# Performance work log

Hardware: AMD Instinct MI355X
Metric: run time of the kernel (lower is better)

Reference implementation:

```python
import jax, jax.numpy as jnp
import numpy as np

V = 50000      # node_num
E = 200000     # number of edges
LN = 128       # feat_dim
S = 32         # stat_dim
C = 10         # num_class
T = 2          # propagation steps
MU = 0.9


def setup_inputs() -> dict:
    key = jax.random.key(0)
    ks = jax.random.split(key, 10)
    feat_Matrix = jax.random.normal(ks[0], (V, LN), dtype=jnp.float32)
    X_Node = jax.random.randint(ks[1], (E,), 0, V, dtype=jnp.int32)
    X_Neis = jax.random.randint(ks[2], (E,), 0, V, dtype=jnp.int32)
    # degrees >= 1 (divided by in Hw)
    dg_list = jax.random.randint(ks[3], (E,), 1, 33).astype(jnp.float32)
    sc = 0.02
    Wxi = jax.random.normal(ks[4], (2 * LN, S * S), dtype=jnp.float32) * sc
    bxi = jnp.zeros((S * S,), dtype=jnp.float32)
    Wrou = jax.random.normal(ks[5], (LN, S), dtype=jnp.float32) * sc
    brou = jnp.zeros((S,), dtype=jnp.float32)
    Wout = jax.random.normal(ks[6], (S, C), dtype=jnp.float32) * sc
    bout = jnp.zeros((C,), dtype=jnp.float32)
    return {
        "feat_Matrix": feat_Matrix, "X_Node": X_Node, "X_Neis": X_Neis,
        "dg_list": dg_list, "Wxi": Wxi, "bxi": bxi,
        "Wrou": Wrou, "brou": brou, "Wout": Wout, "bout": bout,
    }


def reference(feat_Matrix, X_Node, X_Neis, dg_list,
              Wxi, bxi, Wrou, brou, Wout, bout):
    # Gather endpoint features: X = [feat[u] || feat[v]]  -> [E, 2*LN]
    X = jnp.concatenate(
        (feat_Matrix[X_Node], feat_Matrix[X_Neis]), axis=1)

    # Xi(X): per-edge transition matrix A  [E, S, S], scaled by mu/s/deg
    A = jnp.tanh(X @ Wxi + bxi).reshape(E, S, S)
    A = A * (MU / S) / dg_list[:, None, None]
    # Rou on first chunk (= node features)  [E, S]
    b = jnp.tanh(X[:, :LN] @ Wrou + brou)

    H = jnp.zeros((V, S), dtype=feat_Matrix.dtype)
    for _ in range(T):
        He = H[X_Node]                                  # gather  [E, S]
        He = jnp.einsum('eij,ej->ei', A, He) + b        # per-edge transition
        # scatter-add per node (equivalent to AggrSum's dense mask matmul)
        H = jax.ops.segment_sum(He, X_Node, num_segments=V)

    # dropout is identity at inference
    return jax.nn.log_softmax(H @ Wout + bout, axis=-1)
```

## Files before the change

kernel.cpp:

```cpp
#include <hip/hip_runtime.h>

#define EE 200000
#define VV 50000
#define LN 128
#define KD 256
#define SS 32
#define NN 1024
#define CC 10
#define MUS 0.028125f

typedef short short8_t __attribute__((ext_vector_type(8)));
typedef float f32x4 __attribute__((ext_vector_type(4)));

__device__ __forceinline__ unsigned short f32_to_bf16_rne(float f) {
    union { float f; unsigned u; } x; x.f = f;
    unsigned r = x.u + 0x7FFFu + ((x.u >> 16) & 1u);
    return (unsigned short)(r >> 16);
}

__device__ __forceinline__ float bf16_to_f32(unsigned short h) {
    union { unsigned u; float f; } x; x.u = ((unsigned)h) << 16; return x.f;
}

__device__ __forceinline__ float tanh_fast(float x) {
    float t = __builtin_amdgcn_exp2f(x * 2.885390081777927f);
    return 1.0f - 2.0f * __builtin_amdgcn_rcpf(t + 1.0f);
}

__device__ __forceinline__ float ptanh(float x) {
    float x2 = x * x;
    return x * (27.f + x2) * __builtin_amdgcn_rcpf(27.f + 9.f * x2);
}

__device__ __forceinline__ void load_lds16(const void* g, void* l) {
    __builtin_amdgcn_global_load_lds(
        (const __attribute__((address_space(1))) unsigned int*)g,
        (__attribute__((address_space(3))) unsigned int*)l,
        16, 0, 0);
}

__global__ void k_prep(const float* __restrict__ feat, unsigned short* __restrict__ featB,
                       const float* __restrict__ Wxi, unsigned short* __restrict__ WxiB,
                       const float* __restrict__ bxi, float* __restrict__ bxiT,
                       const int* __restrict__ Xn, int* __restrict__ cnt) {
    int b = blockIdx.x, tid = threadIdx.x;
    if (b < 6250) {
        int idx = b * 256 + tid;
        float4 v = ((const float4*)feat)[idx];
        ushort4 o;
        o.x = f32_to_bf16_rne(v.x); o.y = f32_to_bf16_rne(v.y);
        o.z = f32_to_bf16_rne(v.z); o.w = f32_to_bf16_rne(v.w);
        ((ushort4*)featB)[idx] = o;
    } else if (b < 7274) {
        int idx = (b - 6250) * 256 + tid;
        int k = idx >> 10, ncol = idx & 1023;
        int np = ((ncol & 31) << 5) | (ncol >> 5);
        WxiB[((size_t)(k >> 3) * NN + np) * 8 + (k & 7)] = f32_to_bf16_rne(Wxi[idx]);
    } else if (b == 7274) {
        #pragma unroll
        for (int it = 0; it < 4; ++it) {
            int i = it * 256 + tid;
            bxiT[i] = bxi[(i & 31) * 32 + (i >> 5)];
        }
    } else {
        int e = (b - 7275) * 256 + tid;
        if (e < EE) atomicAdd(&cnt[Xn[e]], 1);
    }
}

__global__ void k_scan1(const int* __restrict__ cnt, int* __restrict__ rowptr,
                        int* __restrict__ bsum) {
    __shared__ int s[256];
    int i = blockIdx.x * 256 + threadIdx.x;
    int x = (i < VV) ? cnt[i] : 0;
    s[threadIdx.x] = x; __syncthreads();
    int v = x;
    #pragma unroll
    for (int off = 1; off < 256; off <<= 1) {
        int t = (threadIdx.x >= off) ? s[threadIdx.x - off] : 0;
        __syncthreads();
        v += t; s[threadIdx.x] = v;
        __syncthreads();
    }
    if (i < VV) rowptr[i] = v - x;
    if (threadIdx.x == 255) bsum[blockIdx.x] = v;
}

__global__ void k_scan2(const int* __restrict__ bsum, int* __restrict__ boff, int nb) {
    __shared__ int s[256];
    int t = threadIdx.x;
    int x = (t < nb) ? bsum[t] : 0;
    s[t] = x; __syncthreads();
    int v = x;
    #pragma unroll
    for (int off = 1; off < 256; off <<= 1) {
        int tt = (t >= off) ? s[t - off] : 0;
        __syncthreads();
        v += tt; s[t] = v;
        __syncthreads();
    }
    boff[t] = v - x;
}

__global__ void k_scan3(int* __restrict__ rowptr, const int* __restrict__ boff,
                        int* __restrict__ cursor) {
    int i = blockIdx.x * 256 + threadIdx.x;
    if (i < VV) {
        int r = rowptr[i] + boff[blockIdx.x];
        rowptr[i] = r;
        cursor[i] = r;
    }
    if (blockIdx.x == 0 && threadIdx.x == 0) rowptr[VV] = EE;
}

__global__ void k_scatter(const int* __restrict__ Xn, int* __restrict__ cursor,
                          int* __restrict__ perm) {
    int e = blockIdx.x * 256 + threadIdx.x;
    if (e < EE) {
        int p = atomicAdd(&cursor[Xn[e]], 1);
        perm[p] = e;
    }
}

__global__ void k_h1(const float* __restrict__ feat, const float* __restrict__ Wrou,
                     const float* __restrict__ brou, const int* __restrict__ cnt,
                     float* __restrict__ H1) {
    int gid = blockIdx.x * 256 + threadIdx.x;
    int u = gid >> 5, s = gid & 31;
    const float* fr = feat + (size_t)u * LN;
    float a = brou[s];
    #pragma unroll 8
    for (int k = 0; k < LN; ++k) a += fr[k] * Wrou[k * SS + s];
    H1[gid] = (float)cnt[u] * tanh_fast(a);
}

__global__ void __launch_bounds__(256, 3)
k_edge_gemm(const unsigned short* __restrict__ featB, const unsigned short* __restrict__ WxiB,
            const int* __restrict__ Xn, const int* __restrict__ Xe,
            const float* __restrict__ dg, const float* __restrict__ bxiT,
            const int* __restrict__ perm, const float* __restrict__ H1,
            unsigned short* __restrict__ HeB) {
    __shared__ __align__(16) unsigned short Bs[2 * 8192];
    __shared__ float hs[128][33];
    __shared__ int   us[128], vs[128];
    __shared__ float scale_s[128];

    const int tid = threadIdx.x;
    const int eb = blockIdx.x * 128;

    if (tid < 128) {
        int p = eb + tid; if (p > EE - 1) p = EE - 1;
        int e0 = perm[p];
        us[tid] = Xn[e0]; vs[tid] = Xe[e0];
        scale_s[tid] = MUS / dg[e0];
    }
    __syncthreads();

    const int w = tid >> 6, lane = tid & 63;
    const int g = lane >> 4, l15 = lane & 15;
    const int row0 = w * 32;

    short8_t af[8][2];
    #pragma unroll
    for (int kk = 0; kk < 8; ++kk)
        #pragma unroll
        for (int mf = 0; mf < 2; ++mf) {
            int el = row0 + mf * 16 + l15;
            int node = (kk < 4) ? us[el] : vs[el];
            af[kk][mf] = *(const short8_t*)(featB + (size_t)node * LN + (kk & 3) * 32 + g * 8);
        }

    #pragma unroll
    for (int it = 0; it < 16; ++it) {
        int idx = it * 256 + tid;
        int el = idx >> 5, s = idx & 31;
        hs[el][s] = H1[us[el] * SS + s];
    }

    size_t qoff[4];
    int ldsoff[4];
    #pragma unroll
    for (int q = 0; q < 4; ++q) {
        int U = q * 256 + tid;
        qoff[q] = (size_t)(U >> 5) * 16384 + (size_t)(U & 31) * 16;
        ldsoff[q] = U * 16;
    }
    const char* bbase = (const char*)Bs + (g * 512 + l15 * 16);

    f32x4 he[2][2];
    #pragma unroll
    for (int mf = 0; mf < 2; ++mf)
        #pragma unroll
        for (int f = 0; f < 2; ++f)
            he[mf][f] = (f32x4){0.f, 0.f, 0.f, 0.f};

    #pragma unroll
    for (int q = 0; q < 4; ++q)
        load_lds16((const char*)WxiB + qoff[q], (char*)Bs + ldsoff[q]);
    __syncthreads();

    #pragma unroll 1
    for (int c = 0; c < 32; ++c) {
        if (c < 31) {
            const char* gs = (const char*)WxiB + (size_t)(c + 1) * 512;
            char* ld = (char*)Bs + ((c + 1) & 1) * 16384;
            #pragma unroll
            for (int q = 0; q < 4; ++q)
                load_lds16(gs + qoff[q], ld + ldsoff[q]);
        }

        const char* bslot = bbase + (c & 1) * 16384;
        f32x4 acc[2][2];
        #pragma unroll
        for (int mf = 0; mf < 2; ++mf)
            #pragma unroll
            for (int f = 0; f < 2; ++f)
                acc[mf][f] = (f32x4){0.f, 0.f, 0.f, 0.f};

        #pragma unroll
        for (int kk = 0; kk < 8; ++kk) {
            short8_t b0 = *(const short8_t*)(bslot + kk * 2048);
            short8_t b1 = *(const short8_t*)(bslot + kk * 2048 + 256);
            #pragma unroll
            for (int mf = 0; mf < 2; ++mf) {
                acc[mf][0] = __builtin_amdgcn_mfma_f32_16x16x32_bf16(af[kk][mf], b0, acc[mf][0], 0, 0, 0);
                acc[mf][1] = __builtin_amdgcn_mfma_f32_16x16x32_bf16(af[kk][mf], b1, acc[mf][1], 0, 0, 0);
            }
        }

        const float bx0 = bxiT[c * 32 + l15];
        const float bx1 = bxiT[c * 32 + 16 + l15];
        #pragma unroll
        for (int mf = 0; mf < 2; ++mf)
            #pragma unroll
            for (int r = 0; r < 4; ++r) {
                float hv = hs[row0 + mf * 16 + g * 4 + r][c];
                he[mf][0][r] += ptanh(acc[mf][0][r] + bx0) * hv;
                he[mf][1][r] += ptanh(acc[mf][1][r] + bx1) * hv;
            }

        __syncthreads();
    }

    #pragma unroll
    for (int mf = 0; mf < 2; ++mf)
        #pragma unroll
        for (int r = 0; r < 4; ++r) {
            int el = row0 + mf * 16 + g * 4 + r;
            int ep = eb + el;
            if (ep < EE) {
                float sc = scale_s[el];
                HeB[(size_t)ep * SS + l15]      = f32_to_bf16_rne(he[mf][0][r] * sc);
                HeB[(size_t)ep * SS + 16 + l15] = f32_to_bf16_rne(he[mf][1][r] * sc);
            }
        }
}

__global__ void k_reduce_out(const unsigned short* __restrict__ HeB, const int* __restrict__ rowptr,
                             const float* __restrict__ H1, const float* __restrict__ Wout,
                             const float* __restrict__ bout, float* __restrict__ out) {
    __shared__ float h2[8][33];
    __shared__ float lgS[8][10];
    __shared__ float lseS[8];
    int tid = threadIdx.x;
    int un8 = tid >> 5, s = tid & 31;
    int u = blockIdx.x * 8 + un8;
    int p0 = rowptr[u], p1 = rowptr[u + 1];
    float acc = H1[u * SS + s];
    for (int p = p0; p < p1; ++p)
        acc += bf16_to_f32(HeB[(size_t)p * SS + s]);
    h2[un8][s] = acc;
    __syncthreads();
    if (tid < 80) {
        int un = tid / 10, c = tid - un * 10;
        float a = bout[c];
        #pragma unroll
        for (int s2 = 0; s2 < SS; ++s2) a += h2[un][s2] * Wout[s2 * CC + c];
        lgS[un][c] = a;
    }
    __syncthreads();
    if (tid < 8) {
        float mx = lgS[tid][0];
        #pragma unroll
        for (int c = 1; c < CC; ++c) mx = fmaxf(mx, lgS[tid][c]);
        float se = 0.f;
        #pragma unroll
        for (int c = 0; c < CC; ++c)
            se += __builtin_amdgcn_exp2f((lgS[tid][c] - mx) * 1.4426950408889634f);
        lseS[tid] = mx + __builtin_amdgcn_logf(se) * 0.6931471805599453f;
    }
    __syncthreads();
    if (tid < 80) {
        int un = tid / 10, c = tid - un * 10;
        out[(size_t)(blockIdx.x * 8 + un) * CC + c] = lgS[un][c] - lseS[un];
    }
}

extern "C" void kernel_launch(void* const* d_in, const int* in_sizes, int n_in,
                              void* d_out, int out_size, void* d_ws, size_t ws_size,
                              hipStream_t stream) {
    const float* feat = (const float*)d_in[0];
    const int*   Xn   = (const int*)d_in[1];
    const int*   Xe   = (const int*)d_in[2];
    const float* dg   = (const float*)d_in[3];
    const float* Wxi  = (const float*)d_in[4];
    const float* bxi  = (const float*)d_in[5];
    const float* Wrou = (const float*)d_in[6];
    const float* brou = (const float*)d_in[7];
    const float* Wout = (const float*)d_in[8];
    const float* bout = (const float*)d_in[9];
    float* out = (float*)d_out;

    char* ws = (char*)d_ws;
    unsigned short* featB  = (unsigned short*)(ws);
    unsigned short* WxiB   = (unsigned short*)(ws + 12800000);
    unsigned short* HeB    = (unsigned short*)(ws + 13324288);
    float*          H1     = (float*)(ws + 26124288);
    int*            perm   = (int*)(ws + 32524288);
    int*            rowptr = (int*)(ws + 33324288);
    int*            cursor = (int*)(ws + 33524352);
    int*            cnt    = (int*)(ws + 33724352);
    float*          bxiT   = (float*)(ws + 33924352);
    int*            bsum   = (int*)(ws + 33928448);
    int*            boff   = (int*)(ws + 33929472);

    hipMemsetAsync(cnt, 0, 200000, stream);

    k_prep      <<<8057, 256, 0, stream>>>(feat, featB, Wxi, WxiB, bxi, bxiT, Xn, cnt);
    k_h1        <<<(VV * SS) / 256, 256, 0, stream>>>(feat, Wrou, brou, cnt, H1);
    k_scan1     <<<196, 256, 0, stream>>>(cnt, rowptr, bsum);
    k_scan2     <<<1, 256, 0, stream>>>(bsum, boff, 196);
    k_scan3     <<<196, 256, 0, stream>>>(rowptr, boff, cursor);
    k_scatter   <<<782, 256, 0, stream>>>(Xn, cursor, perm);
    k_edge_gemm <<<(EE + 127) / 128, 256, 0, stream>>>(featB, WxiB, Xn, Xe, dg, bxiT, perm, H1, HeB);
    k_reduce_out<<<VV / 8, 256, 0, stream>>>(HeB, rowptr, H1, Wout, bout, out);
}
```

Before: 322.4 us.

## Fuse rou into prep, single-pass lookback scan, and double edge tile per block

Moves the Rou projection into the prep kernel, storing tanh(feat@Wrou) without the degree factor; the degree is now recovered from rowptr where it is used. The three-kernel scan becomes one decoupled-lookback scan that publishes block flags through a zeroed workspace. The edge GEMM now handles 256 edges per block with four M-fragments per wave and launch bounds lowered to two blocks. It also replaces the loop-end __syncthreads with an explicit waitcnt and barrier. The aim is fewer launches and more reuse of each Wxi tile loaded into LDS, at the cost of more registers and lower occupancy, plus a lookback that relies on blocks being scheduled in order.

```diff
diff --git a/kernel.cpp b/kernel.cpp
--- a/kernel.cpp
+++ b/kernel.cpp
@@ -42,7 +42,9 @@
 __global__ void k_prep(const float* __restrict__ feat, unsigned short* __restrict__ featB,
                        const float* __restrict__ Wxi, unsigned short* __restrict__ WxiB,
                        const float* __restrict__ bxi, float* __restrict__ bxiT,
-                       const int* __restrict__ Xn, int* __restrict__ cnt) {
+                       const int* __restrict__ Xn, int* __restrict__ cnt,
+                       const float* __restrict__ Wrou, const float* __restrict__ brou,
+                       float* __restrict__ R) {
     int b = blockIdx.x, tid = threadIdx.x;
     if (b < 6250) {
         int idx = b * 256 + tid;
@@ -62,55 +64,81 @@
             int i = it * 256 + tid;
             bxiT[i] = bxi[(i & 31) * 32 + (i >> 5)];
         }
-    } else {
+    } else if (b < 8057) {
         int e = (b - 7275) * 256 + tid;
         if (e < EE) atomicAdd(&cnt[Xn[e]], 1);
-    }
-}
-
-__global__ void k_scan1(const int* __restrict__ cnt, int* __restrict__ rowptr,
-                        int* __restrict__ bsum) {
+    } else {
+        int gid = (b - 8057) * 256 + tid;
+        int u = gid >> 5, s = gid & 31;
+        const float* fr = feat + (size_t)u * LN;
+        float a = brou[s];
+        #pragma unroll 8
+        for (int k = 0; k < LN; ++k) a += fr[k] * Wrou[k * SS + s];
+        R[gid] = tanh_fast(a);
+    }
+}
+
+__global__ void __launch_bounds__(256) k_scan_lb(const int* __restrict__ cnt,
+                                                 int* __restrict__ rowptr,
+                                                 int* __restrict__ cursor,
+                                                 unsigned int* flags) {
     __shared__ int s[256];
-    int i = blockIdx.x * 256 + threadIdx.x;
+    __shared__ int bp;
+    int b = blockIdx.x, tid = threadIdx.x;
+    int i = b * 256 + tid;
     int x = (i < VV) ? cnt[i] : 0;
-    s[threadIdx.x] = x; __syncthreads();
+    s[tid] = x; __syncthreads();
     int v = x;
     #pragma unroll
     for (int off = 1; off < 256; off <<= 1) {
-        int t = (threadIdx.x >= off) ? s[threadIdx.x - off] : 0;
+        int t = (tid >= off) ? s[tid - off] : 0;
         __syncthreads();
-        v += t; s[threadIdx.x] = v;
+        v += t; s[tid] = v;
         __syncthreads();
     }
-    if (i < VV) rowptr[i] = v - x;
-    if (threadIdx.x == 255) bsum[blockIdx.x] = v;
-}
-
-__global__ void k_scan2(const int* __restrict__ bsum, int* __restrict__ boff, int nb) {
-    __shared__ int s[256];
-    int t = threadIdx.x;
-    int x = (t < nb) ? bsum[t] : 0;
-    s[t] = x; __syncthreads();
-    int v = x;
-    #pragma unroll
-    for (int off = 1; off < 256; off <<= 1) {
-        int tt = (t >= off) ? s[t - off] : 0;
-        __syncthreads();
-        v += tt; s[t] = v;
-        __syncthreads();
-    }
-    boff[t] = v - x;
-}
-
-__global__ void k_scan3(int* __restrict__ rowptr, const int* __restrict__ boff,
-                        int* __restrict__ cursor) {
-    int i = blockIdx.x * 256 + threadIdx.x;
-    if (i < VV) {
-        int r = rowptr[i] + boff[blockIdx.x];
-        rowptr[i] = r;
-        cursor[i] = r;
-    }
-    if (blockIdx.x == 0 && threadIdx.x == 0) rowptr[VV] = EE;
+    int agg = s[255];
+
+    if (b == 0) {
+        if (tid == 0) {
+            bp = 0;
+            atomicExch(&flags[0], 0x80000000u | (unsigned)agg);
+        }
+    } else {
+        if (tid == 0)
+            atomicExch(&flags[b], 0x40000000u | (unsigned)agg);
+        if (tid < 64) {
+            int lane = tid;
+            int base = b - 1;
+            int pref = 0;
+            while (true) {
+                int idx = base - lane;
+                unsigned wv;
+                if (idx >= 0) {
+                    do { wv = atomicAdd(&flags[idx], 0u); } while ((wv & 0xC0000000u) == 0u);
+                } else {
+                    wv = 0x80000000u;
+                }
+                bool isP = (wv >= 0x80000000u);
+                unsigned long long bal = __ballot(isP);
+                int Lp = bal ? __builtin_ctzll(bal) : 64;
+                int val = (int)(wv & 0x3FFFFFFFu);
+                int contrib = (lane < Lp) ? val : ((lane == Lp && bal) ? val : 0);
+                #pragma unroll
+                for (int o = 1; o < 64; o <<= 1) contrib += __shfl_xor(contrib, o);
+                pref += contrib;
+                if (bal) break;
+                base -= 64;
+            }
+            if (lane == 0) {
+                bp = pref;
+                atomicExch(&flags[b], 0x80000000u | (unsigned)(pref + agg));
+            }
+        }
+    }
+    __syncthreads();
+    int excl = v - x + bp;
+    if (i < VV) { rowptr[i] = excl; cursor[i] = excl; }
+    if (b == 0 && tid == 0) rowptr[VV] = EE;
 }
 
 __global__ void k_scatter(const int* __restrict__ Xn, int* __restrict__ cursor,
@@ -122,59 +150,49 @@
     }
 }
 
-__global__ void k_h1(const float* __restrict__ feat, const float* __restrict__ Wrou,
-                     const float* __restrict__ brou, const int* __restrict__ cnt,
-                     float* __restrict__ H1) {
-    int gid = blockIdx.x * 256 + threadIdx.x;
-    int u = gid >> 5, s = gid & 31;
-    const float* fr = feat + (size_t)u * LN;
-    float a = brou[s];
-    #pragma unroll 8
-    for (int k = 0; k < LN; ++k) a += fr[k] * Wrou[k * SS + s];
-    H1[gid] = (float)cnt[u] * tanh_fast(a);
-}
-
-__global__ void __launch_bounds__(256, 3)
+__global__ void __launch_bounds__(256, 2)
 k_edge_gemm(const unsigned short* __restrict__ featB, const unsigned short* __restrict__ WxiB,
             const int* __restrict__ Xn, const int* __restrict__ Xe,
             const float* __restrict__ dg, const float* __restrict__ bxiT,
-            const int* __restrict__ perm, const float* __restrict__ H1,
-            unsigned short* __restrict__ HeB) {
+            const int* __restrict__ perm, const float* __restrict__ R,
+            const int* __restrict__ rowptr, unsigned short* __restrict__ HeB) {
     __shared__ __align__(16) unsigned short Bs[2 * 8192];
-    __shared__ float hs[128][33];
-    __shared__ int   us[128], vs[128];
-    __shared__ float scale_s[128];
+    __shared__ float hs[256][33];
+    __shared__ int   us[256], vs[256];
+    __shared__ float scale_s[256], cs[256];
 
     const int tid = threadIdx.x;
-    const int eb = blockIdx.x * 128;
-
-    if (tid < 128) {
+    const int eb = blockIdx.x * 256;
+
+    {
         int p = eb + tid; if (p > EE - 1) p = EE - 1;
         int e0 = perm[p];
-        us[tid] = Xn[e0]; vs[tid] = Xe[e0];
+        int u = Xn[e0];
+        us[tid] = u; vs[tid] = Xe[e0];
         scale_s[tid] = MUS / dg[e0];
+        cs[tid] = (float)(rowptr[u + 1] - rowptr[u]);
     }
     __syncthreads();
 
     const int w = tid >> 6, lane = tid & 63;
     const int g = lane >> 4, l15 = lane & 15;
-    const int row0 = w * 32;
-
-    short8_t af[8][2];
+    const int row0 = w * 64;
+
+    short8_t af[8][4];
     #pragma unroll
     for (int kk = 0; kk < 8; ++kk)
         #pragma unroll
-        for (int mf = 0; mf < 2; ++mf) {
+        for (int mf = 0; mf < 4; ++mf) {
             int el = row0 + mf * 16 + l15;
             int node = (kk < 4) ? us[el] : vs[el];
             af[kk][mf] = *(const short8_t*)(featB + (size_t)node * LN + (kk & 3) * 32 + g * 8);
         }
 
     #pragma unroll
-    for (int it = 0; it < 16; ++it) {
+    for (int it = 0; it < 32; ++it) {
         int idx = it * 256 + tid;
-        int el = idx >> 5, s = idx & 31;
-        hs[el][s] = H1[us[el] * SS + s];
+        int el = idx >> 5, s2 = idx & 31;
+        hs[el][s2] = cs[el] * R[us[el] * SS + s2];
     }
 
     size_t qoff[4];
@@ -187,9 +205,9 @@
     }
     const char* bbase = (const char*)Bs + (g * 512 + l15 * 16);
 
-    f32x4 he[2][2];
-    #pragma unroll
-    for (int mf = 0; mf < 2; ++mf)
+    f32x4 he[4][2];
+    #pragma unroll
+    for (int mf = 0; mf < 4; ++mf)
         #pragma unroll
         for (int f = 0; f < 2; ++f)
             he[mf][f] = (f32x4){0.f, 0.f, 0.f, 0.f};
@@ -210,9 +228,9 @@
         }
 
         const char* bslot = bbase + (c & 1) * 16384;
-        f32x4 acc[2][2];
-        #pragma unroll
-        for (int mf = 0; mf < 2; ++mf)
+        f32x4 acc[4][2];
+        #pragma unroll
+        for (int mf = 0; mf < 4; ++mf)
             #pragma unroll
             for (int f = 0; f < 2; ++f)
                 acc[mf][f] = (f32x4){0.f, 0.f, 0.f, 0.f};
@@ -222,7 +240,7 @@
             short8_t b0 = *(const short8_t*)(bslot + kk * 2048);
             short8_t b1 = *(const short8_t*)(bslot + kk * 2048 + 256);
             #pragma unroll
-            for (int mf = 0; mf < 2; ++mf) {
+            for (int mf = 0; mf < 4; ++mf) {
                 acc[mf][0] = __builtin_amdgcn_mfma_f32_16x16x32_bf16(af[kk][mf], b0, acc[mf][0], 0, 0, 0);
                 acc[mf][1] = __builtin_amdgcn_mfma_f32_16x16x32_bf16(af[kk][mf], b1, acc[mf][1], 0, 0, 0);
             }
@@ -231,7 +249,7 @@
         const float bx0 = bxiT[c * 32 + l15];
         const float bx1 = bxiT[c * 32 + 16 + l15];
         #pragma unroll
-        for (int mf = 0; mf < 2; ++mf)
+        for (int mf = 0; mf < 4; ++mf)
             #pragma unroll
             for (int r = 0; r < 4; ++r) {
                 float hv = hs[row0 + mf * 16 + g * 4 + r][c];
@@ -239,11 +257,13 @@
                 he[mf][1][r] += ptanh(acc[mf][1][r] + bx1) * hv;
             }
 
-        __syncthreads();
-    }
-
-    #pragma unroll
-    for (int mf = 0; mf < 2; ++mf)
+        asm volatile("s_waitcnt vmcnt(0)" ::: "memory");
+        __builtin_amdgcn_s_barrier();
+        __builtin_amdgcn_sched_barrier(0);
+    }
+
+    #pragma unroll
+    for (int mf = 0; mf < 4; ++mf)
         #pragma unroll
         for (int r = 0; r < 4; ++r) {
             int el = row0 + mf * 16 + g * 4 + r;
@@ -257,7 +277,7 @@
 }
 
 __global__ void k_reduce_out(const unsigned short* __restrict__ HeB, const int* __restrict__ rowptr,
-                             const float* __restrict__ H1, const float* __restrict__ Wout,
+                             const float* __restrict__ R, const float* __restrict__ Wout,
                              const float* __restrict__ bout, float* __restrict__ out) {
     __shared__ float h2[8][33];
     __shared__ float lgS[8][10];
@@ -266,7 +286,7 @@
     int un8 = tid >> 5, s = tid & 31;
     int u = blockIdx.x * 8 + un8;
     int p0 = rowptr[u], p1 = rowptr[u + 1];
-    float acc = H1[u * SS + s];
+    float acc = (float)(p1 - p0) * R[u * SS + s];
     for (int p = p0; p < p1; ++p)
         acc += bf16_to_f32(HeB[(size_t)p * SS + s]);
     h2[un8][s] = acc;
@@ -315,23 +335,20 @@
     unsigned short* featB  = (unsigned short*)(ws);
     unsigned short* WxiB   = (unsigned short*)(ws + 12800000);
     unsigned short* HeB    = (unsigned short*)(ws + 13324288);
-    float*          H1     = (float*)(ws + 26124288);
+    float*          R      = (float*)(ws + 26124288);
     int*            perm   = (int*)(ws + 32524288);
     int*            rowptr = (int*)(ws + 33324288);
     int*            cursor = (int*)(ws + 33524352);
     int*            cnt    = (int*)(ws + 33724352);
-    float*          bxiT   = (float*)(ws + 33924352);
-    int*            bsum   = (int*)(ws + 33928448);
-    int*            boff   = (int*)(ws + 33929472);
-
-    hipMemsetAsync(cnt, 0, 200000, stream);
-
-    k_prep      <<<8057, 256, 0, stream>>>(feat, featB, Wxi, WxiB, bxi, bxiT, Xn, cnt);
-    k_h1        <<<(VV * SS) / 256, 256, 0, stream>>>(feat, Wrou, brou, cnt, H1);
-    k_scan1     <<<196, 256, 0, stream>>>(cnt, rowptr, bsum);
-    k_scan2     <<<1, 256, 0, stream>>>(bsum, boff, 196);
-    k_scan3     <<<196, 256, 0, stream>>>(rowptr, boff, cursor);
+    unsigned int*   flags  = (unsigned int*)(ws + 33924352);
+    float*          bxiT   = (float*)(ws + 33925376);
+
+    hipMemsetAsync(cnt, 0, 201024, stream);
+
+    k_prep      <<<14307, 256, 0, stream>>>(feat, featB, Wxi, WxiB, bxi, bxiT, Xn, cnt,
+                                            Wrou, brou, R);
+    k_scan_lb   <<<196, 256, 0, stream>>>(cnt, rowptr, cursor, flags);
     k_scatter   <<<782, 256, 0, stream>>>(Xn, cursor, perm);
-    k_edge_gemm <<<(EE + 127) / 128, 256, 0, stream>>>(featB, WxiB, Xn, Xe, dg, bxiT, perm, H1, HeB);
-    k_reduce_out<<<VV / 8, 256, 0, stream>>>(HeB, rowptr, H1, Wout, bout, out);
-}
+    k_edge_gemm <<<782, 256, 0, stream>>>(featB, WxiB, Xn, Xe, dg, bxiT, perm, R, rowptr, HeB);
+    k_reduce_out<<<VV / 8, 256, 0, stream>>>(HeB, rowptr, R, Wout, bout, out);
+}
```

After: 319.7 us. Within noise of the previous version (-0.8%).
